# Kernel optimization log

Hardware: AMD Instinct MI355X
Metric: run time of the kernel (lower is better)

The kernel has to match this reference:

```python
import jax, jax.numpy as jnp
import numpy as np

Q_CHAN = 8          # q_chan
IN_CHAN = 128
KS = 56             # kernel_size; ks*ks must equal h*w
STRIDE = 2
BN_EPS = 1e-5


def setup_inputs() -> dict:
    key = jax.random.key(0)
    ks = jax.random.split(key, 10)
    n, c, h, w = 4, IN_CHAN, 56, 56
    hw = h * w  # 3136 == KS*KS
    oc = 4 * Q_CHAN  # qkv conv output channels = 32
    return {
        "x": jax.random.normal(ks[0], (n, c, h, w), dtype=jnp.float32),
        # 1x1 conv weight (out_ch, in_ch) and bias
        "w_qkv": jax.random.normal(ks[1], (oc, c), dtype=jnp.float32) * (1.0 / np.sqrt(c)),
        "b_qkv": jnp.zeros((oc,), dtype=jnp.float32),
        # BatchNorm (inference mode) affine + running stats
        "bn_gamma": jnp.ones((oc,), dtype=jnp.float32),
        "bn_beta": jnp.zeros((oc,), dtype=jnp.float32),
        "bn_mean": jnp.zeros((oc,), dtype=jnp.float32),
        "bn_var": jnp.ones((oc,), dtype=jnp.float32),
        # learned relative position biases, trailing dim = ks*ks = h*w
        "rq": jax.random.normal(ks[2], (Q_CHAN, KS * KS), dtype=jnp.float32),
        "rk": jax.random.normal(ks[3], (Q_CHAN, KS * KS), dtype=jnp.float32),
        "rv": jax.random.normal(ks[4], (2 * Q_CHAN, KS * KS), dtype=jnp.float32),
    }


def reference(x, w_qkv, b_qkv, bn_gamma, bn_beta, bn_mean, bn_var, rq, rk, rv):
    n, c, h, w = x.shape
    # 1x1 conv + inference BatchNorm
    qkv = jnp.einsum('nchw,oc->nohw', x, w_qkv) + b_qkv[None, :, None, None]
    scale = bn_gamma / jnp.sqrt(bn_var + BN_EPS)
    qkv = (qkv - bn_mean[None, :, None, None]) * scale[None, :, None, None] + bn_beta[None, :, None, None]
    qkv = qkv.reshape(n, 4 * Q_CHAN, h * w)
    q = qkv[:, :Q_CHAN]            # [n, 8, hw]
    k = qkv[:, Q_CHAN:2 * Q_CHAN]  # [n, 8, hw]
    v = qkv[:, 2 * Q_CHAN:]        # [n, 16, hw]
    # global attention scores with learned positional bias terms: [n, hw, hw]
    sc = (jnp.einsum('nci,ncj->nij', q, k)
          + jnp.einsum('ci,ncj->nij', rq, q)
          + jnp.einsum('ci,ncj->nij', rk, k))
    sc = jax.nn.softmax(sc, axis=2)
    v = v + rv[None]
    out = jnp.einsum('nij,ncj->nci', sc, v).reshape(n, 2 * Q_CHAN, h, w)
    # AvgPool2d(kernel=stride, stride=stride)
    s = STRIDE
    out = out.reshape(n, 2 * Q_CHAN, h // s, s, w // s, s).mean(axis=(3, 5))
    return out
```

## Files before the change

### kernel.cpp

```cpp
#include <hip/hip_runtime.h>

#define HW 3136
#define CIN 128
#define MHAT 40.0f
#define NSEV 7
#define LOG2E 1.44269504088896340736f
#define NEGC  (-57.7078018f)

typedef __attribute__((ext_vector_type(8))) short bf16x8;
typedef __attribute__((ext_vector_type(4))) float f32x4;

__device__ __forceinline__ unsigned cvtpk(float a, float b) {
    unsigned r;
    asm("v_cvt_pk_bf16_f32 %0, %1, %2" : "=v"(r) : "v"(a), "v"(b));
    return r;
}
__device__ __forceinline__ float lo2f(unsigned p) { return __uint_as_float(p << 16); }
__device__ __forceinline__ float hi2f(unsigned p) { return __uint_as_float(p & 0xffff0000u); }
__device__ __forceinline__ float exp2_hw(float x) {
    float r;
    asm("v_exp_f32 %0, %1" : "=v"(r) : "v"(x));
    return r;
}
__device__ __forceinline__ void pl32(unsigned &a, unsigned &b) {
    asm("v_permlane32_swap_b32 %0, %1" : "+v"(a), "+v"(b));
}
__device__ __forceinline__ void pl16(unsigned &a, unsigned &b) {
    asm("v_permlane16_swap_b32 %0, %1" : "+v"(a), "+v"(b));
}

union UF { bf16x8 v; unsigned u[4]; };


__global__ __launch_bounds__(64) void proj_mfma(
    const float* __restrict__ x, const float* __restrict__ w,
    const float* __restrict__ bq, const float* __restrict__ gm,
    const float* __restrict__ bt, const float* __restrict__ mu,
    const float* __restrict__ vr, const float* __restrict__ rq,
    const float* __restrict__ rk, const float* __restrict__ rv,
    short* __restrict__ QKWS, short* __restrict__ ASQB, short* __restrict__ VWS)
{
    const int lane = threadIdx.x;
    const int il = lane & 15, q = lane >> 4;
    const int jb = blockIdx.x * 16;
    const int nn = blockIdx.y;
    const int jA = jb + il;
    const float* xn = x + (size_t)nn * CIN * HW;

    UF xh[4], xl[4];
    #pragma unroll
    for (int s = 0; s < 4; ++s) {
        float xv[8];
        #pragma unroll
        for (int u = 0; u < 8; ++u)
            xv[u] = xn[(size_t)(s * 32 + q * 8 + u) * HW + jA];
        #pragma unroll
        for (int t = 0; t < 4; ++t) {
            unsigned hp = cvtpk(xv[2 * t], xv[2 * t + 1]);
            unsigned lp = cvtpk(xv[2 * t] - lo2f(hp), xv[2 * t + 1] - hi2f(hp));
            xh[s].u[t] = hp;
            xl[s].u[t] = lp;
        }
    }
    UF wh0[4], wl0[4], wh1[4], wl1[4];
    {
        const float* wp0 = w + (size_t)il * CIN;
        const float* wp1 = w + (size_t)(16 + il) * CIN;
        #pragma unroll
        for (int s = 0; s < 4; ++s) {
            float4 f0 = *(const float4*)(wp0 + s * 32 + q * 8);
            float4 f1 = *(const float4*)(wp0 + s * 32 + q * 8 + 4);
            float g0[8] = {f0.x, f0.y, f0.z, f0.w, f1.x, f1.y, f1.z, f1.w};
            float4 h0 = *(const float4*)(wp1 + s * 32 + q * 8);
            float4 h1 = *(const float4*)(wp1 + s * 32 + q * 8 + 4);
            float g1[8] = {h0.x, h0.y, h0.z, h0.w, h1.x, h1.y, h1.z, h1.w};
            #pragma unroll
            for (int t = 0; t < 4; ++t) {
                unsigned hp0 = cvtpk(g0[2 * t], g0[2 * t + 1]);
                unsigned lp0 = cvtpk(g0[2 * t] - lo2f(hp0), g0[2 * t + 1] - hi2f(hp0));
                wh0[s].u[t] = hp0;
                wl0[s].u[t] = lp0;
                unsigned hp1 = cvtpk(g1[2 * t], g1[2 * t + 1]);
                unsigned lp1 = cvtpk(g1[2 * t] - lo2f(hp1), g1[2 * t + 1] - hi2f(hp1));
                wh1[s].u[t] = hp1;
                wl1[s].u[t] = lp1;
            }
        }
    }

    f32x4 a0 = {0.f, 0.f, 0.f, 0.f}, a1 = {0.f, 0.f, 0.f, 0.f};
    #pragma unroll
    for (int s = 0; s < 4; ++s) a0 = __builtin_amdgcn_mfma_f32_16x16x32_bf16(wh0[s].v, xh[s].v, a0, 0, 0, 0);
    #pragma unroll
    for (int s = 0; s < 4; ++s) a1 = __builtin_amdgcn_mfma_f32_16x16x32_bf16(wl0[s].v, xh[s].v, a1, 0, 0, 0);
    #pragma unroll
    for (int s = 0; s < 4; ++s) a1 = __builtin_amdgcn_mfma_f32_16x16x32_bf16(wh0[s].v, xl[s].v, a1, 0, 0, 0);
    const f32x4 d0 = a0 + a1;
    f32x4 b0 = {0.f, 0.f, 0.f, 0.f}, b1 = {0.f, 0.f, 0.f, 0.f};
    #pragma unroll
    for (int s = 0; s < 4; ++s) b0 = __builtin_amdgcn_mfma_f32_16x16x32_bf16(xh[s].v, wh1[s].v, b0, 0, 0, 0);
    #pragma unroll
    for (int s = 0; s < 4; ++s) b1 = __builtin_amdgcn_mfma_f32_16x16x32_bf16(xl[s].v, wh1[s].v, b1, 0, 0, 0);
    #pragma unroll
    for (int s = 0; s < 4; ++s) b1 = __builtin_amdgcn_mfma_f32_16x16x32_bf16(xh[s].v, wl1[s].v, b1, 0, 0, 0);
    const f32x4 d1 = b0 + b1;

    {
        const int jj = jA;
        float hv[4], av[4];
        #pragma unroll
        for (int r = 0; r < 4; ++r) {
            const int ch = q * 4 + r;
            const float sc = gm[ch] * rsqrtf(vr[ch] + 1e-5f);
            const float sh = (bq[ch] - mu[ch]) * sc + bt[ch];
            const float val = d0[r] * sc + sh;
            hv[r] = val;
            const float a = (ch < 8) ? (val + rk[(size_t)ch * HW + jj])
                                     : rq[(size_t)(ch - 8) * HW + jj];
            av[r] = a * LOG2E;
        }
        short* qrow = QKWS + ((size_t)nn * HW + jj) * 32;
        short* arow = ASQB + ((size_t)nn * HW + jj) * 32;
        const int pb = (q * 4) ^ 8;
        unsigned h01 = cvtpk(hv[0], hv[1]), h23 = cvtpk(hv[2], hv[3]);
        unsigned l01 = cvtpk(hv[0] - lo2f(h01), hv[1] - hi2f(h01));
        unsigned l23 = cvtpk(hv[2] - lo2f(h23), hv[3] - hi2f(h23));
        *(unsigned*)&qrow[pb]          = h01;
        *(unsigned*)&qrow[pb + 2]      = h23;
        *(unsigned*)&qrow[16 + pb]     = l01;
        *(unsigned*)&qrow[16 + pb + 2] = l23;
        unsigned c01 = cvtpk(av[0], av[1]), c23 = cvtpk(av[2], av[3]);
        unsigned e01 = cvtpk(av[0] - lo2f(c01), av[1] - hi2f(c01));
        unsigned e23 = cvtpk(av[2] - lo2f(c23), av[3] - hi2f(c23));
        *(unsigned*)&arow[q * 4]          = c01;
        *(unsigned*)&arow[q * 4 + 2]      = c23;
        *(unsigned*)&arow[16 + q * 4]     = e01;
        *(unsigned*)&arow[16 + q * 4 + 2] = e23;
    }
    {
        const int ch = 16 + il;
        const float sc = gm[ch] * rsqrtf(vr[ch] + 1e-5f);
        const float sh = (bq[ch] - mu[ch]) * sc + bt[ch];
        const int jbase = jb + q * 4;
        float4 rvv = *(const float4*)(rv + (size_t)il * HW + jbase);
        float v0 = d1[0] * sc + sh + rvv.x;
        float v1 = d1[1] * sc + sh + rvv.y;
        float v2 = d1[2] * sc + sh + rvv.z;
        float v3 = d1[3] * sc + sh + rvv.w;
        short* vp = VWS + (size_t)(nn * 16 + il) * HW + jbase;
        *(unsigned*)&vp[0] = cvtpk(v0, v1);
        *(unsigned*)&vp[2] = cvtpk(v2, v3);
    }
}

#define JT 224
#define QKS 40
#define VTS 232

__global__ __launch_bounds__(256) void attn_mfma(
    const short* __restrict__ QKWS, const short* __restrict__ ASQB,
    const short* __restrict__ VWS,
    float* __restrict__ ONUM, float* __restrict__ OLS)
{
    __shared__ short QK[JT * QKS];
    __shared__ short VT[16 * VTS];
    const int tid = threadIdx.x;
    const int wv = tid >> 6, lane = tid & 63;
    const int il = lane & 15, q = lane >> 4;
    const int b   = blockIdx.x;
    const int sev = b / 196;
    const int ig  = b % 196;
    const int nn  = ig / 49;
    const int tile = (ig % 49) * 4 + wv;
    const int i0  = tile * 16;

    const bf16x8 bco = *(const bf16x8*)(ASQB + ((size_t)nn * HW + i0 + il) * 32 + q * 8);
    const bf16x8 zero8 = {0, 0, 0, 0, 0, 0, 0, 0};
    const bf16x8 bco2 = (q < 2) ? bco : zero8;

    const f32x4 DINIT = {NEGC, NEGC, NEGC, NEGC};
    f32x4 outc = {0.f, 0.f, 0.f, 0.f};
    float lsum = 0.f;

    const int jb0 = (sev * 2 + 0) * JT;
    const int jb1 = (sev * 2 + 1) * JT;
    const int c_v = tid >> 4, jg = tid & 15;

    int4 qa0, qa1, qa2, qa3;
    unsigned vt0, vt1, vt2, vt3, vt4, vt5, vt6;

    if (tid < JT) {
        const short* src = QKWS + ((size_t)nn * HW + jb0 + tid) * 32;
        qa0 = *(const int4*)(src);
        qa1 = *(const int4*)(src + 8);
        qa2 = *(const int4*)(src + 16);
        qa3 = *(const int4*)(src + 24);
    }
    {
        const unsigned* vs = (const unsigned*)(VWS + (size_t)(nn * 16 + c_v) * HW + jb0 + jg * 14);
        vt0 = vs[0]; vt1 = vs[1]; vt2 = vs[2]; vt3 = vs[3]; vt4 = vs[4]; vt5 = vs[5]; vt6 = vs[6];
    }
    if (tid < JT) {
        short* row = &QK[tid * QKS];
        *(int4*)&row[0]  = qa0;
        *(int4*)&row[8]  = qa1;
        *(int4*)&row[16] = qa2;
        *(int4*)&row[24] = qa3;
    }
    {
        unsigned* vd = (unsigned*)&VT[c_v * VTS + jg * 14];
        vd[0] = vt0; vd[1] = vt1; vd[2] = vt2; vd[3] = vt3; vd[4] = vt4; vd[5] = vt5; vd[6] = vt6;
    }
    __syncthreads();

    if (tid < JT) {
        const short* src = QKWS + ((size_t)nn * HW + jb1 + tid) * 32;
        qa0 = *(const int4*)(src);
        qa1 = *(const int4*)(src + 8);
        qa2 = *(const int4*)(src + 16);
        qa3 = *(const int4*)(src + 24);
    }
    {
        const unsigned* vs = (const unsigned*)(VWS + (size_t)(nn * 16 + c_v) * HW + jb1 + jg * 14);
        vt0 = vs[0]; vt1 = vs[1]; vt2 = vs[2]; vt3 = vs[3]; vt4 = vs[4]; vt5 = vs[5]; vt6 = vs[6];
    }

    auto compute7 = [&]() {
        #pragma unroll
        for (int pr = 0; pr < 7; ++pr) {
            unsigned E0, E1, O0, O1;
            {
                const short* arow = &QK[((2 * pr) * 16 + il) * QKS + (q & 1) * 8];
                bf16x8 a1 = *(const bf16x8*)arow;
                bf16x8 a2 = *(const bf16x8*)(arow + 16);
                __builtin_amdgcn_s_setprio(1);
                f32x4 d = __builtin_amdgcn_mfma_f32_16x16x32_bf16(a1, bco, DINIT, 0, 0, 0);
                d = __builtin_amdgcn_mfma_f32_16x16x32_bf16(a2, bco2, d, 0, 0, 0);
                __builtin_amdgcn_s_setprio(0);
                float p0 = exp2_hw(d[0]), p1 = exp2_hw(d[1]);
                float p2 = exp2_hw(d[2]), p3 = exp2_hw(d[3]);
                lsum += (p0 + p1) + (p2 + p3);
                E0 = cvtpk(p0, p1); E1 = cvtpk(p2, p3);
            }
            {
                const short* arow = &QK[((2 * pr + 1) * 16 + il) * QKS + (q & 1) * 8];
                bf16x8 a1 = *(const bf16x8*)arow;
                bf16x8 a2 = *(const bf16x8*)(arow + 16);
                __builtin_amdgcn_s_setprio(1);
                f32x4 d = __builtin_amdgcn_mfma_f32_16x16x32_bf16(a1, bco, DINIT, 0, 0, 0);
                d = __builtin_amdgcn_mfma_f32_16x16x32_bf16(a2, bco2, d, 0, 0, 0);
                __builtin_amdgcn_s_setprio(0);
                float p0 = exp2_hw(d[0]), p1 = exp2_hw(d[1]);
                float p2 = exp2_hw(d[2]), p3 = exp2_hw(d[3]);
                lsum += (p0 + p1) + (p2 + p3);
                O0 = cvtpk(p0, p1); O1 = cvtpk(p2, p3);
            }
            pl32(E0, O0); pl32(E1, O1);
            pl16(E0, O0); pl16(E1, O1);
            UF ap; ap.u[0] = E0; ap.u[1] = E1; ap.u[2] = O0; ap.u[3] = O1;
            bf16x8 bv = *(const bf16x8*)&VT[il * VTS + pr * 32 + q * 8];
            __builtin_amdgcn_s_setprio(1);
            outc = __builtin_amdgcn_mfma_f32_16x16x32_bf16(ap.v, bv, outc, 0, 0, 0);
            __builtin_amdgcn_s_setprio(0);
        }
    };

    compute7();
    __syncthreads();

    if (tid < JT) {
        short* row = &QK[tid * QKS];
        *(int4*)&row[0]  = qa0;
        *(int4*)&row[8]  = qa1;
        *(int4*)&row[16] = qa2;
        *(int4*)&row[24] = qa3;
    }
    {
        unsigned* vd = (unsigned*)&VT[c_v * VTS + jg * 14];
        vd[0] = vt0; vd[1] = vt1; vd[2] = vt2; vd[3] = vt3; vd[4] = vt4; vd[5] = vt5; vd[6] = vt6;
    }
    __syncthreads();

    compute7();

    lsum += __shfl_xor(lsum, 16);
    lsum += __shfl_xor(lsum, 32);
    float* np = ONUM + ((size_t)(sev * 4 + nn) * 196 + tile) * 256;
    *(f32x4*)(np + il * 16 + q * 4) = outc;
    if (lane < 16)
        OLS[(size_t)(sev * 4 + nn) * HW + i0 + lane] = lsum;
}

__global__ __launch_bounds__(256) void pool_kernel(
    const float* __restrict__ ONUM, const float* __restrict__ OLS,
    float* __restrict__ out)
{
    __shared__ float LI[112];
    __shared__ float PL[2][16][28];
    const int tid = threadIdx.x;
    const int oh  = blockIdx.x;
    const int nn  = blockIdx.y;
    const int T0  = 7 * oh;

    if (tid < 112) {
        float l = 0.f;
        #pragma unroll
        for (int p = 0; p < NSEV; ++p)
            l += OLS[(size_t)(p * 4 + nn) * HW + 112 * oh + tid];
        LI[tid] = l;
    }
    __syncthreads();

    const int c  = tid >> 4;
    const int u0 = tid & 15;
    for (int u = u0; u < 28; u += 16) {
        const int tt = u >> 2, qd = u & 3;
        const int o  = u * 4;
        float4 nu = {0.f, 0.f, 0.f, 0.f};
        #pragma unroll
        for (int p = 0; p < NSEV; ++p) {
            const float4 v = *(const float4*)(ONUM +
                ((size_t)(p * 4 + nn) * 196 + T0 + tt) * 256 + c * 16 + qd * 4);
            nu.x += v.x; nu.y += v.y; nu.z += v.z; nu.w += v.w;
        }
        const float r0 = nu.x / LI[o], r1 = nu.y / LI[o + 1];
        const float r2 = nu.z / LI[o + 2], r3 = nu.w / LI[o + 3];
        const int hb = o / 56, wo = o % 56;
        PL[hb][c][wo >> 1]       = r0 + r1;
        PL[hb][c][(wo >> 1) + 1] = r2 + r3;
    }
    __syncthreads();

    for (int v = tid; v < 448; v += 256) {
        const int cc = v / 28, wo = v % 28;
        out[((nn * 16 + cc) * 28 + oh) * 28 + wo] = 0.25f * (PL[0][cc][wo] + PL[1][cc][wo]);
    }
}

#define FJC 392
#define FPSTR 394

__global__ __launch_bounds__(512, 2) void fused_attn(
    const float* __restrict__ x, const float* __restrict__ w,
    const float* __restrict__ bq, const float* __restrict__ gm,
    const float* __restrict__ bt, const float* __restrict__ mu,
    const float* __restrict__ vr, const float* __restrict__ rq,
    const float* __restrict__ rk, const float* __restrict__ rv,
    float* __restrict__ out)
{
    __shared__ float PT[32][FPSTR];
    __shared__ float SQ[56][16];
    __shared__ float ST[56][17];

    const int tid  = threadIdx.x;
    const int wv   = tid >> 6, lane = tid & 63;
    const int bid  = blockIdx.x;
    const int nn   = bid / 56, rem = bid % 56;
    const int oh   = rem >> 1, half = rem & 1;
    const float* xn = x + (size_t)nn * CIN * HW;

    if (tid < 448) {
        int r = tid >> 3, c = tid & 7;
        int rh = (r >= 28) ? 1 : 0, rw = r - 28*rh;
        int i  = (2*oh + rh)*56 + half*28 + rw;
        float acc = 0.f;
        for (int cc = 0; cc < CIN; ++cc)
            acc += xn[cc*HW + i] * w[c*CIN + cc];
        float s  = gm[c] * rsqrtf(vr[c] + 1e-5f);
        float qv = (acc + bq[c] - mu[c])*s + bt[c];
        SQ[r][c]   = qv + rk[c*HW + i];
        SQ[r][8+c] = rq[c*HW + i];
    }

    float l_[7];
    float ac_[7][16];
    #pragma unroll
    for (int r = 0; r < 7; ++r) {
        l_[r] = 0.f;
        #pragma unroll
        for (int c = 0; c < 16; ++c) ac_[r][c] = 0.f;
    }
    __syncthreads();

    for (int cb = 0; cb < 8; ++cb) {
        const int jbase = cb * FJC;
        const int o0 = wv * 4;
        for (int t = 0; t < 4; ++t) {
            int p = lane + 64*t;
            if (p < 196) {
                int j0 = jbase + 2*p;
                float a0x=0.f,a0y=0.f,a1x=0.f,a1y=0.f,a2x=0.f,a2y=0.f,a3x=0.f,a3y=0.f;
                for (int cc = 0; cc < CIN; ++cc) {
                    float2 xv = *(const float2*)(xn + (size_t)cc*HW + j0);
                    float w0 = w[(o0+0)*CIN + cc];
                    float w1 = w[(o0+1)*CIN + cc];
                    float w2 = w[(o0+2)*CIN + cc];
                    float w3 = w[(o0+3)*CIN + cc];
                    a0x += xv.x*w0; a0y += xv.y*w0;
                    a1x += xv.x*w1; a1y += xv.y*w1;
                    a2x += xv.x*w2; a2y += xv.y*w2;
                    a3x += xv.x*w3; a3y += xv.y*w3;
                }
                #pragma unroll
                for (int u = 0; u < 4; ++u) {
                    int o = o0 + u;
                    float av0 = (u==0)? a0x : (u==1)? a1x : (u==2)? a2x : a3x;
                    float av1 = (u==0)? a0y : (u==1)? a1y : (u==2)? a2y : a3y;
                    float s  = gm[o] * rsqrtf(vr[o] + 1e-5f);
                    float sh = (bq[o] - mu[o])*s + bt[o];
                    float v0 = av0*s + sh, v1 = av1*s + sh;
                    if (o >= 16) {
                        v0 += rv[(o-16)*HW + j0];
                        v1 += rv[(o-16)*HW + j0 + 1];
                    }
                    *(float2*)&PT[o][2*p] = make_float2(v0, v1);
                }
            }
        }
        __syncthreads();

        #pragma unroll
        for (int rr = 0; rr < 7; rr += 2) {
            const bool two = (rr + 1) < 7;
            const int ra = wv*7 + rr;
            float A1a[8], A2a[8], A1b[8], A2b[8];
            #pragma unroll
            for (int c = 0; c < 8; ++c) {
                A1a[c] = SQ[ra][c];   A2a[c] = SQ[ra][8+c];
                A1b[c] = two ? SQ[ra+1][c]   : 0.f;
                A2b[c] = two ? SQ[ra+1][8+c] : 0.f;
            }
            for (int t = 0; t < 7; ++t) {
                int jl = 64*t + lane;
                if (jl < FJC) {
                    float qv[8], kv[8], vv[16];
                    #pragma unroll
                    for (int c = 0; c < 8; ++c) { qv[c] = PT[c][jl]; kv[c] = PT[8+c][jl]; }
                    #pragma unroll
                    for (int c = 0; c < 16; ++c) vv[c] = PT[16+c][jl];
                    float sa = 0.f, sb = 0.f;
                    #pragma unroll
                    for (int c = 0; c < 8; ++c) {
                        sa += A1a[c]*kv[c] + A2a[c]*qv[c];
                        sb += A1b[c]*kv[c] + A2b[c]*qv[c];
                    }
                    float pa = __expf(sa - MHAT);
                    l_[rr] += pa;
                    #pragma unroll
                    for (int c = 0; c < 16; ++c) ac_[rr][c] += pa * vv[c];
                    if (two) {
                        float pb = __expf(sb - MHAT);
                        l_[rr+1] += pb;
                        #pragma unroll
                        for (int c = 0; c < 16; ++c) ac_[rr+1][c] += pb * vv[c];
                    }
                }
            }
        }
        __syncthreads();
    }

    #pragma unroll
    for (int rr = 0; rr < 7; ++rr) {
        int r = wv*7 + rr;
        float l = l_[rr];
        #pragma unroll
        for (int off = 32; off; off >>= 1) l += __shfl_xor(l, off);
        if (lane == 0) ST[r][16] = l;
        #pragma unroll
        for (int c = 0; c < 16; ++c) {
            float a = ac_[rr][c];
            #pragma unroll
            for (int off = 32; off; off >>= 1) a += __shfl_xor(a, off);
            if (lane == c) ST[r][c] = a;
        }
    }
    __syncthreads();

    if (tid < 224) {
        int c = tid & 15, qq = tid >> 4;
        float s = 0.f;
        #pragma unroll
        for (int rh = 0; rh < 2; ++rh)
            #pragma unroll
            for (int dw = 0; dw < 2; ++dw) {
                int r = rh*28 + 2*qq + dw;
                s += ST[r][c] / ST[r][16];
            }
        out[((nn*16 + c)*28 + oh)*28 + half*14 + qq] = 0.25f * s;
    }
}

extern "C" void kernel_launch(void* const* d_in, const int* in_sizes, int n_in,
                              void* d_out, int out_size, void* d_ws, size_t ws_size,
                              hipStream_t stream) {
    const float* x     = (const float*)d_in[0];
    const float* w     = (const float*)d_in[1];
    const float* bq    = (const float*)d_in[2];
    const float* gm    = (const float*)d_in[3];
    const float* bt    = (const float*)d_in[4];
    const float* mu    = (const float*)d_in[5];
    const float* vr    = (const float*)d_in[6];
    const float* rq    = (const float*)d_in[7];
    const float* rk    = (const float*)d_in[8];
    const float* rv    = (const float*)d_in[9];
    float* out = (float*)d_out;

    const size_t ONF = (size_t)NSEV * 4 * 196 * 256;
    const size_t OLF = (size_t)NSEV * 4 * HW;
    const size_t QKF = (size_t)4 * HW * 32;
    const size_t VWF = (size_t)4 * 16 * HW;
    const size_t NEED = (ONF + OLF) * sizeof(float) + (2 * QKF + VWF) * sizeof(short);

    if (ws_size >= NEED) {
        float* ONUM = (float*)d_ws;
        float* OLS  = ONUM + ONF;
        short* QKWS = (short*)(OLS + OLF);
        short* ASQB = QKWS + QKF;
        short* VWS  = ASQB + QKF;
        proj_mfma<<<dim3(196, 4), 64, 0, stream>>>(x, w, bq, gm, bt, mu, vr, rq, rk, rv, QKWS, ASQB, VWS);
        attn_mfma<<<dim3(196 * NSEV), 256, 0, stream>>>(QKWS, ASQB, VWS, ONUM, OLS);
        pool_kernel<<<dim3(28, 4), 256, 0, stream>>>(ONUM, OLS, out);
    } else {
        fused_attn<<<dim3(224), dim3(512), 0, stream>>>(x, w, bq, gm, bt, mu, vr, rq, rk, rv, out);
    }
}
```

Baseline: 97.58 us.

## Process two query tiles per attention block to reuse staged K/V

Each attention block now computes two 16-row query tiles per wave (paired as g and 48-g), so the QK and V tiles staged in shared memory are reused twice and the grid shrinks from 196 to 100 blocks per key chunk. This is meant to cut per-tile global loads, LDS staging and barrier overhead, and to give independent MFMA chains for better latency hiding. It raises register pressure and adds a divergent single-tile path for the middle group.

```diff
diff --git a/kernel.cpp b/kernel.cpp
--- a/kernel.cpp
+++ b/kernel.cpp
@@ -168,19 +168,28 @@
     const int wv = tid >> 6, lane = tid & 63;
     const int il = lane & 15, q = lane >> 4;
     const int b   = blockIdx.x;
-    const int sev = b / 196;
-    const int ig  = b % 196;
-    const int nn  = ig / 49;
-    const int tile = (ig % 49) * 4 + wv;
-    const int i0  = tile * 16;
-
-    const bf16x8 bco = *(const bf16x8*)(ASQB + ((size_t)nn * HW + i0 + il) * 32 + q * 8);
+    const int sev = b / 100;
+    const int rem = b % 100;
+    const int nn  = rem / 25;
+    const int g   = rem % 25;
+    const bool dual = (g < 24);
+    const int tileA = g * 4 + wv;
+    const int tileB = (48 - g) * 4 + wv;
+    const int i0A = tileA * 16;
+    const int i0B = tileB * 16;
+
+    const bf16x8 bcoA = *(const bf16x8*)(ASQB + ((size_t)nn * HW + i0A + il) * 32 + q * 8);
     const bf16x8 zero8 = {0, 0, 0, 0, 0, 0, 0, 0};
-    const bf16x8 bco2 = (q < 2) ? bco : zero8;
+    const bf16x8 bco2A = (q < 2) ? bcoA : zero8;
+    bf16x8 bcoB = zero8, bco2B = zero8;
+    if (dual) {
+        bcoB = *(const bf16x8*)(ASQB + ((size_t)nn * HW + i0B + il) * 32 + q * 8);
+        bco2B = (q < 2) ? bcoB : zero8;
+    }
 
     const f32x4 DINIT = {NEGC, NEGC, NEGC, NEGC};
-    f32x4 outc = {0.f, 0.f, 0.f, 0.f};
-    float lsum = 0.f;
+    f32x4 outcA = {0.f, 0.f, 0.f, 0.f}, outcB = {0.f, 0.f, 0.f, 0.f};
+    float lsumA = 0.f, lsumB = 0.f;
 
     const int jb0 = (sev * 2 + 0) * JT;
     const int jb1 = (sev * 2 + 1) * JT;
@@ -228,40 +237,72 @@
     auto compute7 = [&]() {
         #pragma unroll
         for (int pr = 0; pr < 7; ++pr) {
-            unsigned E0, E1, O0, O1;
+            unsigned EA0, EA1, OA0, OA1, EB0, EB1, OB0, OB1;
             {
                 const short* arow = &QK[((2 * pr) * 16 + il) * QKS + (q & 1) * 8];
                 bf16x8 a1 = *(const bf16x8*)arow;
                 bf16x8 a2 = *(const bf16x8*)(arow + 16);
                 __builtin_amdgcn_s_setprio(1);
-                f32x4 d = __builtin_amdgcn_mfma_f32_16x16x32_bf16(a1, bco, DINIT, 0, 0, 0);
-                d = __builtin_amdgcn_mfma_f32_16x16x32_bf16(a2, bco2, d, 0, 0, 0);
+                f32x4 dA = __builtin_amdgcn_mfma_f32_16x16x32_bf16(a1, bcoA, DINIT, 0, 0, 0);
+                dA = __builtin_amdgcn_mfma_f32_16x16x32_bf16(a2, bco2A, dA, 0, 0, 0);
+                f32x4 dB;
+                if (dual) {
+                    dB = __builtin_amdgcn_mfma_f32_16x16x32_bf16(a1, bcoB, DINIT, 0, 0, 0);
+                    dB = __builtin_amdgcn_mfma_f32_16x16x32_bf16(a2, bco2B, dB, 0, 0, 0);
+                }
                 __builtin_amdgcn_s_setprio(0);
-                float p0 = exp2_hw(d[0]), p1 = exp2_hw(d[1]);
-                float p2 = exp2_hw(d[2]), p3 = exp2_hw(d[3]);
-                lsum += (p0 + p1) + (p2 + p3);
-                E0 = cvtpk(p0, p1); E1 = cvtpk(p2, p3);
+                float p0 = exp2_hw(dA[0]), p1 = exp2_hw(dA[1]);
+                float p2 = exp2_hw(dA[2]), p3 = exp2_hw(dA[3]);
+                lsumA += (p0 + p1) + (p2 + p3);
+                EA0 = cvtpk(p0, p1); EA1 = cvtpk(p2, p3);
+                if (dual) {
+                    float b0 = exp2_hw(dB[0]), b1 = exp2_hw(dB[1]);
+                    float b2 = exp2_hw(dB[2]), b3 = exp2_hw(dB[3]);
+                    lsumB += (b0 + b1) + (b2 + b3);
+                    EB0 = cvtpk(b0, b1); EB1 = cvtpk(b2, b3);
+                }
             }
             {
                 const short* arow = &QK[((2 * pr + 1) * 16 + il) * QKS + (q & 1) * 8];
                 bf16x8 a1 = *(const bf16x8*)arow;
                 bf16x8 a2 = *(const bf16x8*)(arow + 16);
                 __builtin_amdgcn_s_setprio(1);
-                f32x4 d = __builtin_amdgcn_mfma_f32_16x16x32_bf16(a1, bco, DINIT, 0, 0, 0);
-                d = __builtin_amdgcn_mfma_f32_16x16x32_bf16(a2, bco2, d, 0, 0, 0);
+                f32x4 dA = __builtin_amdgcn_mfma_f32_16x16x32_bf16(a1, bcoA, DINIT, 0, 0, 0);
+                dA = __builtin_amdgcn_mfma_f32_16x16x32_bf16(a2, bco2A, dA, 0, 0, 0);
+                f32x4 dB;
+                if (dual) {
+                    dB = __builtin_amdgcn_mfma_f32_16x16x32_bf16(a1, bcoB, DINIT, 0, 0, 0);
+                    dB = __builtin_amdgcn_mfma_f32_16x16x32_bf16(a2, bco2B, dB, 0, 0, 0);
+                }
                 __builtin_amdgcn_s_setprio(0);
-                float p0 = exp2_hw(d[0]), p1 = exp2_hw(d[1]);
-                float p2 = exp2_hw(d[2]), p3 = exp2_hw(d[3]);
-                lsum += (p0 + p1) + (p2 + p3);
-                O0 = cvtpk(p0, p1); O1 = cvtpk(p2, p3);
-            }
-            pl32(E0, O0); pl32(E1, O1);
-            pl16(E0, O0); pl16(E1, O1);
-            UF ap; ap.u[0] = E0; ap.u[1] = E1; ap.u[2] = O0; ap.u[3] = O1;
+                float p0 = exp2_hw(dA[0]), p1 = exp2_hw(dA[1]);
+                float p2 = exp2_hw(dA[2]), p3 = exp2_hw(dA[3]);
+                lsumA += (p0 + p1) + (p2 + p3);
+                OA0 = cvtpk(p0, p1); OA1 = cvtpk(p2, p3);
+                if (dual) {
+                    float b0 = exp2_hw(dB[0]), b1 = exp2_hw(dB[1]);
+                    float b2 = exp2_hw(dB[2]), b3 = exp2_hw(dB[3]);
+                    lsumB += (b0 + b1) + (b2 + b3);
+                    OB0 = cvtpk(b0, b1); OB1 = cvtpk(b2, b3);
+                }
+            }
+            pl32(EA0, OA0); pl32(EA1, OA1);
+            pl16(EA0, OA0); pl16(EA1, OA1);
+            UF apA; apA.u[0] = EA0; apA.u[1] = EA1; apA.u[2] = OA0; apA.u[3] = OA1;
             bf16x8 bv = *(const bf16x8*)&VT[il * VTS + pr * 32 + q * 8];
-            __builtin_amdgcn_s_setprio(1);
-            outc = __builtin_amdgcn_mfma_f32_16x16x32_bf16(ap.v, bv, outc, 0, 0, 0);
-            __builtin_amdgcn_s_setprio(0);
+            if (dual) {
+                pl32(EB0, OB0); pl32(EB1, OB1);
+                pl16(EB0, OB0); pl16(EB1, OB1);
+                UF apB; apB.u[0] = EB0; apB.u[1] = EB1; apB.u[2] = OB0; apB.u[3] = OB1;
+                __builtin_amdgcn_s_setprio(1);
+                outcA = __builtin_amdgcn_mfma_f32_16x16x32_bf16(apA.v, bv, outcA, 0, 0, 0);
+                outcB = __builtin_amdgcn_mfma_f32_16x16x32_bf16(apB.v, bv, outcB, 0, 0, 0);
+                __builtin_amdgcn_s_setprio(0);
+            } else {
+                __builtin_amdgcn_s_setprio(1);
+                outcA = __builtin_amdgcn_mfma_f32_16x16x32_bf16(apA.v, bv, outcA, 0, 0, 0);
+                __builtin_amdgcn_s_setprio(0);
+            }
         }
     };
 
@@ -283,12 +324,20 @@
 
     compute7();
 
-    lsum += __shfl_xor(lsum, 16);
-    lsum += __shfl_xor(lsum, 32);
-    float* np = ONUM + ((size_t)(sev * 4 + nn) * 196 + tile) * 256;
-    *(f32x4*)(np + il * 16 + q * 4) = outc;
+    lsumA += __shfl_xor(lsumA, 16);
+    lsumA += __shfl_xor(lsumA, 32);
+    float* npA = ONUM + ((size_t)(sev * 4 + nn) * 196 + tileA) * 256;
+    *(f32x4*)(npA + il * 16 + q * 4) = outcA;
     if (lane < 16)
-        OLS[(size_t)(sev * 4 + nn) * HW + i0 + lane] = lsum;
+        OLS[(size_t)(sev * 4 + nn) * HW + i0A + lane] = lsumA;
+    if (dual) {
+        lsumB += __shfl_xor(lsumB, 16);
+        lsumB += __shfl_xor(lsumB, 32);
+        float* npB = ONUM + ((size_t)(sev * 4 + nn) * 196 + tileB) * 256;
+        *(f32x4*)(npB + il * 16 + q * 4) = outcB;
+        if (lane < 16)
+            OLS[(size_t)(sev * 4 + nn) * HW + i0B + lane] = lsumB;
+    }
 }
 
 __global__ __launch_bounds__(256) void pool_kernel(
@@ -519,7 +568,7 @@
         short* ASQB = QKWS + QKF;
         short* VWS  = ASQB + QKF;
         proj_mfma<<<dim3(196, 4), 64, 0, stream>>>(x, w, bq, gm, bt, mu, vr, rq, rk, rv, QKWS, ASQB, VWS);
-        attn_mfma<<<dim3(196 * NSEV), 256, 0, stream>>>(QKWS, ASQB, VWS, ONUM, OLS);
+        attn_mfma<<<dim3(100 * NSEV), 256, 0, stream>>>(QKWS, ASQB, VWS, ONUM, OLS);
         pool_kernel<<<dim3(28, 4), 256, 0, stream>>>(ONUM, OLS, out);
     } else {
         fused_attn<<<dim3(224), dim3(512), 0, stream>>>(x, w, bq, gm, bt, mu, vr, rq, rk, rv, out);
```

Measured after the change: 101.3 us. 1.04x slower.
